# Kernel tuning notes

Measured on AMD Instinct MI355X. Metric: run time of the kernel, lower is better.

## Reference

```python
import jax, jax.numpy as jnp
import numpy as np

B, SQ, SK, DIMG, DTXT, D, H = 512, 49, 50, 2048, 768, 512, 4
DH = D // H
LN_EPS = 1e-5


def _proj_head(x, W1, b1, W2, b2, g, be):
    # Linear -> GELU -> Linear -> residual -> LayerNorm (dropout = eval/no-op)
    p = x @ W1 + b1
    h = jax.nn.gelu(p, approximate=False) @ W2 + b2 + p
    mu = h.mean(-1, keepdims=True)
    var = ((h - mu) ** 2).mean(-1, keepdims=True)
    return g * (h - mu) * jax.lax.rsqrt(var + LN_EPS) + be


def setup_inputs() -> dict:
    key = jax.random.key(0)
    ks = jax.random.split(key, 12)
    s = 0.02
    inp = {
        'image_features': jax.random.normal(ks[0], (B, DIMG, SQ), jnp.float32),
        'text_embeddings': jax.random.normal(ks[1], (B, SK, DTXT), jnp.float32),
        # image projection head (2048 -> 512)
        'Wi1': jax.random.normal(ks[2], (DIMG, D), jnp.float32) * s,
        'bi1': jnp.zeros((D,), jnp.float32),
        'Wi2': jax.random.normal(ks[3], (D, D), jnp.float32) * s,
        'bi2': jnp.zeros((D,), jnp.float32),
        'gi': jnp.ones((D,), jnp.float32),
        'bei': jnp.zeros((D,), jnp.float32),
        # text projection head (768 -> 512)
        'Wt1': jax.random.normal(ks[4], (DTXT, D), jnp.float32) * s,
        'bt1': jnp.zeros((D,), jnp.float32),
        'Wt2': jax.random.normal(ks[5], (D, D), jnp.float32) * s,
        'bt2': jnp.zeros((D,), jnp.float32),
        'gt': jnp.ones((D,), jnp.float32),
        'bet': jnp.zeros((D,), jnp.float32),
        # multihead cross-attention (embed_dim=512, 4 heads)
        'Wq': jax.random.normal(ks[6], (D, D), jnp.float32) * s,
        'bq': jnp.zeros((D,), jnp.float32),
        'Wk': jax.random.normal(ks[7], (D, D), jnp.float32) * s,
        'bk': jnp.zeros((D,), jnp.float32),
        'Wv': jax.random.normal(ks[8], (D, D), jnp.float32) * s,
        'bv': jnp.zeros((D,), jnp.float32),
        'Wo': jax.random.normal(ks[9], (D, D), jnp.float32) * s,
        'bo': jnp.zeros((D,), jnp.float32),
    }
    return inp


def reference(image_features, text_embeddings,
              Wi1, bi1, Wi2, bi2, gi, bei,
              Wt1, bt1, Wt2, bt2, gt, bet,
              Wq, bq, Wk, bk, Wv, bv, Wo, bo):
    img = jnp.transpose(image_features, (0, 2, 1))          # [B,SQ,2048]
    pi = _proj_head(img, Wi1, bi1, Wi2, bi2, gi, bei)        # [B,SQ,D]
    pt = _proj_head(text_embeddings, Wt1, bt1, Wt2, bt2, gt, bet)  # [B,SK,D]

    # cross attention: query = image tokens, key/value = text tokens
    q = (pi @ Wq + bq).reshape(B, SQ, H, DH)
    k = (pt @ Wk + bk).reshape(B, SK, H, DH)
    v = (pt @ Wv + bv).reshape(B, SK, H, DH)
    scores = jnp.einsum('bqhd,bkhd->bhqk', q, k) * (1.0 / np.sqrt(DH))
    a = jax.nn.softmax(scores, axis=-1)                      # [B,H,SQ,SK]
    o = jnp.einsum('bhqk,bkhd->bqhd', a, v).reshape(B, SQ, D)
    attn_output = o @ Wo + bo                                # [B,SQ,D]
    attn_weights = a.mean(axis=1)                            # torch MHA averages heads

    avg_attn = attn_output.mean(axis=1)                      # AdaptiveAvgPool1d(1) over SQ
    cls = pt[:, 0, :]                                        # [B,D]

    # cosine-similarity matrix: one normalize + matmul replaces B*B kernel launches
    n1 = avg_attn / jnp.linalg.norm(avg_attn, axis=-1, keepdims=True)
    n2 = cls / jnp.linalg.norm(cls, axis=-1, keepdims=True)
    score = n1 @ n2.T                                        # [B,B]
    return (score, attn_output, attn_weights, pi, pt)
```

## Files before the change

### kernel.cpp

```cpp
#include <hip/hip_runtime.h>
#include <math.h>

#define B_    512
#define SQ_   49
#define SK_   50
#define DIMG_ 2048
#define DTXT_ 768
#define D_    512
#define H_    4
#define DH_   128

#define SCORE_OFF 0
#define AO_OFF    262144
#define AW_OFF    13107200
#define PI_OFF    14361600
#define PT_OFF    27206656

typedef unsigned short bfbits;
typedef __attribute__((ext_vector_type(8))) short short8;
typedef __attribute__((ext_vector_type(4))) float floatx4;

static __device__ __forceinline__ bfbits f2bf(float f) {
    union { float f; unsigned u; } a; a.f = f;
    return (bfbits)((a.u + 0x7fffu + ((a.u >> 16) & 1u)) >> 16);
}
static __device__ __forceinline__ float bf2f(bfbits b) {
    union { unsigned u; float f; } a; a.u = ((unsigned)b) << 16;
    return a.f;
}
static __device__ __forceinline__ float gelu_exact(float x) {
    return 0.5f * x * (1.0f + erff(x * 0.70710678118654752f));
}

__global__ __launch_bounds__(256) void wcast_t(
    const float* __restrict__ W, bfbits* __restrict__ Wt, int K, int N)
{
    __shared__ float t[32][33];
    const int k0 = blockIdx.x * 32, n0 = blockIdx.y * 32;
    const int tx = threadIdx.x & 31, ty = threadIdx.x >> 5;
    #pragma unroll
    for (int i = 0; i < 32; i += 8)
        t[ty + i][tx] = W[(size_t)(k0 + ty + i) * N + n0 + tx];
    __syncthreads();
    #pragma unroll
    for (int i = 0; i < 32; i += 8)
        Wt[(size_t)(n0 + ty + i) * K + k0 + tx] = f2bf(t[tx][ty + i]);
}

__global__ __launch_bounds__(256) void img_t(
    const float* __restrict__ img, bfbits* __restrict__ A)
{
    __shared__ float t[64][50];
    const int b = blockIdx.y, k0 = blockIdx.x * 64;
    const float* src = img + (size_t)b * (DIMG_ * SQ_) + (size_t)k0 * SQ_;
    for (int e = threadIdx.x; e < 64 * 49; e += 256) {
        int kl = e / 49, s = e - kl * 49;
        t[kl][s] = src[kl * 49 + s];
    }
    __syncthreads();
    bfbits* dst = A + (size_t)b * SQ_ * DIMG_ + k0;
    for (int e = threadIdx.x; e < 49 * 64; e += 256) {
        int s = e >> 6, kl = e & 63;
        dst[(size_t)s * DIMG_ + kl] = f2bf(t[kl][s]);
    }
}

__global__ __launch_bounds__(256) void cast4(
    const float* __restrict__ x, bfbits* __restrict__ y, int n4)
{
    int i = blockIdx.x * 256 + threadIdx.x;
    if (i < n4) {
        float4 v = ((const float4*)x)[i];
        ushort4 u;
        u.x = f2bf(v.x); u.y = f2bf(v.y); u.z = f2bf(v.z); u.w = f2bf(v.w);
        ((ushort4*)y)[i] = u;
    }
}

template<bool RES, bool GELU, bool WF32, bool WBF>
__global__ __launch_bounds__(256) void gemm_bf16(
    const bfbits* __restrict__ A, const bfbits* __restrict__ Bt,
    const float* __restrict__ bias, const float* res,
    float* Cf, bfbits* __restrict__ Cb, int M, int K)
{
    constexpr int N = 512;
    __shared__ __attribute__((aligned(16))) bfbits As[128 * 32];
    __shared__ __attribute__((aligned(16))) bfbits Bs[128 * 32];
    const int tid  = threadIdx.x;
    const int wave = tid >> 6, lane = tid & 63;
    const int m0 = blockIdx.y * 128, n0 = blockIdx.x * 128;
    const int wm = (wave >> 1) * 64, wn = (wave & 1) * 64;
    const int lr = lane & 15, quad = lane >> 4;

    floatx4 acc[4][4];
    #pragma unroll
    for (int i = 0; i < 4; ++i)
        #pragma unroll
        for (int j = 0; j < 4; ++j) acc[i][j] = 0.0f;

    const int srow = lane >> 2;
    const int skof = (lane & 3) * 8;

    for (int k0 = 0; k0 < K; k0 += 32) {
        #pragma unroll
        for (int i = 0; i < 2; ++i) {
            const int c = wave * 2 + i;
            const int row = c * 16 + srow;
            const bfbits* ga = A + (size_t)(m0 + row) * K + k0 + skof;
            const bfbits* gb = Bt + (size_t)(n0 + row) * K + k0 + skof;
            __builtin_amdgcn_global_load_lds(
                (const __attribute__((address_space(1))) void*)ga,
                (__attribute__((address_space(3))) void*)(As + c * 512), 16, 0, 0);
            __builtin_amdgcn_global_load_lds(
                (const __attribute__((address_space(1))) void*)gb,
                (__attribute__((address_space(3))) void*)(Bs + c * 512), 16, 0, 0);
        }
        __syncthreads();

        short8 af[4], bfv[4];
        #pragma unroll
        for (int i = 0; i < 4; ++i) {
            af[i]  = *(const short8*)(As + (wm + i * 16 + lr) * 32 + quad * 8);
            bfv[i] = *(const short8*)(Bs + (wn + i * 16 + lr) * 32 + quad * 8);
        }
        #pragma unroll
        for (int i = 0; i < 4; ++i)
            #pragma unroll
            for (int j = 0; j < 4; ++j)
                acc[i][j] = __builtin_amdgcn_mfma_f32_16x16x32_bf16(
                    af[i], bfv[j], acc[i][j], 0, 0, 0);
        __syncthreads();
    }

    #pragma unroll
    for (int i = 0; i < 4; ++i) {
        #pragma unroll
        for (int j = 0; j < 4; ++j) {
            const int gc = n0 + wn + j * 16 + lr;
            const float bv = bias[gc];
            #pragma unroll
            for (int r = 0; r < 4; ++r) {
                const int gm = m0 + wm + i * 16 + quad * 4 + r;
                float v = acc[i][j][r] + bv;
                if (RES) v += res[(size_t)gm * N + gc];
                if (WF32) Cf[(size_t)gm * N + gc] = v;
                if (GELU) Cb[(size_t)gm * N + gc] = f2bf(gelu_exact(v));
                else if (WBF) Cb[(size_t)gm * N + gc] = f2bf(v);
            }
        }
    }
}

__global__ __launch_bounds__(256) void ln2_kernel(
    const float* __restrict__ h, const float* __restrict__ g,
    const float* __restrict__ be, float* __restrict__ outf,
    bfbits* __restrict__ outb)
{
    __shared__ float red[256];
    const int row = blockIdx.x;
    const int tid = threadIdx.x;
    float v0 = h[(size_t)row * D_ + tid];
    float v1 = h[(size_t)row * D_ + 256 + tid];
    red[tid] = v0 + v1;
    __syncthreads();
    for (int s = 128; s > 0; s >>= 1) {
        if (tid < s) red[tid] += red[tid + s];
        __syncthreads();
    }
    float mu = red[0] * (1.0f / 512.0f);
    __syncthreads();
    float d0 = v0 - mu, d1 = v1 - mu;
    red[tid] = d0 * d0 + d1 * d1;
    __syncthreads();
    for (int s = 128; s > 0; s >>= 1) {
        if (tid < s) red[tid] += red[tid + s];
        __syncthreads();
    }
    float var = red[0] * (1.0f / 512.0f);
    float sc = rsqrtf(var + 1e-5f);
    float o0 = g[tid] * d0 * sc + be[tid];
    float o1 = g[256 + tid] * d1 * sc + be[256 + tid];
    outf[(size_t)row * D_ + tid]       = o0;
    outf[(size_t)row * D_ + 256 + tid] = o1;
    outb[(size_t)row * D_ + tid]       = f2bf(o0);
    outb[(size_t)row * D_ + 256 + tid] = f2bf(o1);
}

__global__ __launch_bounds__(256) void attn_kernel(
    const bfbits* __restrict__ q, const bfbits* __restrict__ k,
    const bfbits* __restrict__ v, bfbits* __restrict__ o,
    float* __restrict__ aw)
{
    constexpr int ROWF = 69;
    __shared__ float sc[H_][SQ_ * ROWF];
    const int b = blockIdx.x;
    const int tid = threadIdx.x;
    const int h = tid >> 6, lane = tid & 63;
    const int lr = lane & 15, g = lane >> 4;

    const bfbits* kb = k + ((size_t)b * SK_) * D_ + h * DH_;
    const bfbits* qb = q + ((size_t)b * SQ_) * D_ + h * DH_;

    floatx4 acc[4][4];
    #pragma unroll
    for (int mi = 0; mi < 4; ++mi)
        #pragma unroll
        for (int ni = 0; ni < 4; ++ni) acc[mi][ni] = 0.0f;

    #pragma unroll
    for (int ks = 0; ks < 4; ++ks) {
        short8 afr[4], bfr[4];
        #pragma unroll
        for (int mi = 0; mi < 4; ++mi)
            afr[mi] = *(const short8*)(kb + (size_t)(mi * 16 + lr) * D_ + ks * 32 + g * 8);
        #pragma unroll
        for (int ni = 0; ni < 4; ++ni)
            bfr[ni] = *(const short8*)(qb + (size_t)(ni * 16 + lr) * D_ + ks * 32 + g * 8);
        #pragma unroll
        for (int mi = 0; mi < 4; ++mi)
            #pragma unroll
            for (int ni = 0; ni < 4; ++ni)
                acc[mi][ni] = __builtin_amdgcn_mfma_f32_16x16x32_bf16(
                    afr[mi], bfr[ni], acc[mi][ni], 0, 0, 0);
    }

    const float scale = 0.08838834764831845f;
    #pragma unroll
    for (int ni = 0; ni < 4; ++ni) {
        const int qi = ni * 16 + lr;
        float mx = -1e30f;
        #pragma unroll
        for (int mi = 0; mi < 4; ++mi)
            #pragma unroll
            for (int r = 0; r < 4; ++r) {
                const int ki = mi * 16 + g * 4 + r;
                float s = (ki < SK_) ? acc[mi][ni][r] * scale : -1e30f;
                acc[mi][ni][r] = s;
                mx = fmaxf(mx, s);
            }
        mx = fmaxf(mx, __shfl_xor(mx, 16));
        mx = fmaxf(mx, __shfl_xor(mx, 32));
        float sum = 0.f;
        #pragma unroll
        for (int mi = 0; mi < 4; ++mi)
            #pragma unroll
            for (int r = 0; r < 4; ++r) {
                float ev = __expf(acc[mi][ni][r] - mx);
                acc[mi][ni][r] = ev;
                sum += ev;
            }
        sum += __shfl_xor(sum, 16);
        sum += __shfl_xor(sum, 32);
        const float inv = 1.0f / sum;
        if (qi < SQ_) {
            #pragma unroll
            for (int mi = 0; mi < 4; ++mi) {
                float4 w;
                w.x = acc[mi][ni][0] * inv;
                w.y = acc[mi][ni][1] * inv;
                w.z = acc[mi][ni][2] * inv;
                w.w = acc[mi][ni][3] * inv;
                *(float4*)&sc[h][qi * ROWF + mi * 16 + g * 4] = w;
            }
        }
    }
    __syncthreads();

    for (int e = tid; e < SQ_ * SK_; e += 256) {
        int qi = e / SK_, ki = e - qi * SK_;
        const int off = qi * ROWF + ki;
        aw[(size_t)b * (SQ_ * SK_) + e] =
            0.25f * (sc[0][off] + sc[1][off] + sc[2][off] + sc[3][off]);
    }

    const bfbits* vb = v + ((size_t)b * SK_) * D_ + h * DH_;
    bfbits* ob = o + ((size_t)b * SQ_) * D_ + h * DH_;
    for (int e = lane; e < SQ_ * 16; e += 64) {
        const int qi = e >> 4, dc = e & 15;
        const float* sr = &sc[h][qi * ROWF];
        float s[8] = {0.f, 0.f, 0.f, 0.f, 0.f, 0.f, 0.f, 0.f};
        for (int ki = 0; ki < SK_; ++ki) {
            const float a = sr[ki];
            short8 u = *(const short8*)(vb + (size_t)ki * D_ + dc * 8);
            #pragma unroll
            for (int j = 0; j < 8; ++j)
                s[j] = fmaf(a, bf2f((bfbits)u[j]), s[j]);
        }
        short8 ov;
        #pragma unroll
        for (int j = 0; j < 8; ++j) ov[j] = (short)f2bf(s[j]);
        *(short8*)(ob + (size_t)qi * D_ + dc * 8) = ov;
    }
}

__global__ __launch_bounds__(256) void norm_kernel(
    const float* __restrict__ ao, const float* __restrict__ pt,
    float* __restrict__ n1, float* __restrict__ n2)
{
    __shared__ float red[256];
    const int b = blockIdx.x, tid = threadIdx.x;
    float s0 = 0.f, s1 = 0.f;
    for (int s = 0; s < SQ_; ++s) {
        s0 += ao[((size_t)(b * SQ_ + s)) * D_ + tid];
        s1 += ao[((size_t)(b * SQ_ + s)) * D_ + 256 + tid];
    }
    s0 *= (1.0f / 49.0f);
    s1 *= (1.0f / 49.0f);
    red[tid] = s0 * s0 + s1 * s1;
    __syncthreads();
    for (int st = 128; st > 0; st >>= 1) {
        if (tid < st) red[tid] += red[tid + st];
        __syncthreads();
    }
    float inv = rsqrtf(red[0]);
    __syncthreads();
    n1[(size_t)b * D_ + tid] = s0 * inv;
    n1[(size_t)b * D_ + 256 + tid] = s1 * inv;

    float c0 = pt[((size_t)(b * SK_)) * D_ + tid];
    float c1 = pt[((size_t)(b * SK_)) * D_ + 256 + tid];
    red[tid] = c0 * c0 + c1 * c1;
    __syncthreads();
    for (int st = 128; st > 0; st >>= 1) {
        if (tid < st) red[tid] += red[tid + st];
        __syncthreads();
    }
    float inv2 = rsqrtf(red[0]);
    n2[(size_t)b * D_ + tid] = c0 * inv2;
    n2[(size_t)b * D_ + 256 + tid] = c1 * inv2;
}

__global__ __launch_bounds__(256) void score_gemm(
    const float* __restrict__ A, const float* __restrict__ Bm,
    float* __restrict__ C)
{
    const int BM = 64, BN = 64, BK = 16, Kt = 512, Nt = 512;
    __shared__ float As[BK][BM + 1];
    __shared__ float Bs[BK][BN + 1];
    const int tid = threadIdx.x;
    const int m0 = blockIdx.y * BM, n0 = blockIdx.x * BN;
    const int tc = tid & 15, tr = tid >> 4;
    float acc[4][4] = {};
    for (int k0 = 0; k0 < Kt; k0 += BK) {
        #pragma unroll
        for (int i = 0; i < 4; ++i) {
            int idx = tid + i * 256;
            int m = idx >> 4, kk = idx & 15;
            As[kk][m] = A[(size_t)(m0 + m) * Kt + k0 + kk];
            Bs[kk][m] = Bm[(size_t)(n0 + m) * Kt + k0 + kk];
        }
        __syncthreads();
        #pragma unroll
        for (int kk = 0; kk < BK; ++kk) {
            float a4[4], b4[4];
            #pragma unroll
            for (int i = 0; i < 4; ++i) a4[i] = As[kk][tr * 4 + i];
            #pragma unroll
            for (int j = 0; j < 4; ++j) b4[j] = Bs[kk][tc * 4 + j];
            #pragma unroll
            for (int i = 0; i < 4; ++i)
                #pragma unroll
                for (int j = 0; j < 4; ++j)
                    acc[i][j] = fmaf(a4[i], b4[j], acc[i][j]);
        }
        __syncthreads();
    }
    #pragma unroll
    for (int i = 0; i < 4; ++i)
        #pragma unroll
        for (int j = 0; j < 4; ++j)
            C[(size_t)(m0 + tr * 4 + i) * Nt + n0 + tc * 4 + j] = acc[i][j];
}

extern "C" void kernel_launch(void* const* d_in, const int* in_sizes, int n_in,
                              void* d_out, int out_size, void* d_ws, size_t ws_size,
                              hipStream_t stream)
{
    const float* img = (const float*)d_in[0];
    const float* txt = (const float*)d_in[1];
    const float* Wi1 = (const float*)d_in[2];  const float* bi1 = (const float*)d_in[3];
    const float* Wi2 = (const float*)d_in[4];  const float* bi2 = (const float*)d_in[5];
    const float* gi  = (const float*)d_in[6];  const float* bei = (const float*)d_in[7];
    const float* Wt1 = (const float*)d_in[8];  const float* bt1 = (const float*)d_in[9];
    const float* Wt2 = (const float*)d_in[10]; const float* bt2 = (const float*)d_in[11];
    const float* gt  = (const float*)d_in[12]; const float* bet = (const float*)d_in[13];
    const float* Wq  = (const float*)d_in[14]; const float* bq  = (const float*)d_in[15];
    const float* Wk  = (const float*)d_in[16]; const float* bk  = (const float*)d_in[17];
    const float* Wv  = (const float*)d_in[18]; const float* bv  = (const float*)d_in[19];
    const float* Wo  = (const float*)d_in[20]; const float* bo  = (const float*)d_in[21];
    float* out = (float*)d_out;

    bfbits* Wi1T = (bfbits*)d_ws;
    bfbits* Wi2T = Wi1T + 1048576;
    bfbits* Wt1T = Wi2T + 262144;
    bfbits* Wt2T = Wt1T + 393216;
    bfbits* WqT  = Wt2T + 262144;
    bfbits* WkT  = WqT  + 262144;
    bfbits* WvT  = WkT  + 262144;
    bfbits* WoT  = WvT  + 262144;
    bfbits* R1   = WoT  + 262144;
    bfbits* Aimg = R1;
    bfbits* Atxt = R1;
    bfbits* Qbf  = R1 + 20000000;
    bfbits* Kbf  = R1 + 33200000;
    float*  R2   = (float*)(R1 + 51380224);
    bfbits* Vbf  = (bfbits*)R2;
    bfbits* R3   = (bfbits*)(R2 + 13107200);
    bfbits* Obf  = R3;
    bfbits* PiBf = R3 + 13107200;
    bfbits* PtBf = PiBf + 12845056;
    float*  n1   = (float*)(PtBf + 13107200);
    float*  n2   = n1 + 262144;

    const int MI = B_ * SQ_;
    const int MT = B_ * SK_;
    dim3 blk(256);

    wcast_t<<<dim3(DIMG_ / 32, D_ / 32), blk, 0, stream>>>(Wi1, Wi1T, DIMG_, D_);
    wcast_t<<<dim3(D_ / 32, D_ / 32),    blk, 0, stream>>>(Wi2, Wi2T, D_, D_);
    wcast_t<<<dim3(DTXT_ / 32, D_ / 32), blk, 0, stream>>>(Wt1, Wt1T, DTXT_, D_);
    wcast_t<<<dim3(D_ / 32, D_ / 32),    blk, 0, stream>>>(Wt2, Wt2T, D_, D_);
    wcast_t<<<dim3(D_ / 32, D_ / 32),    blk, 0, stream>>>(Wq, WqT, D_, D_);
    wcast_t<<<dim3(D_ / 32, D_ / 32),    blk, 0, stream>>>(Wk, WkT, D_, D_);
    wcast_t<<<dim3(D_ / 32, D_ / 32),    blk, 0, stream>>>(Wv, WvT, D_, D_);
    wcast_t<<<dim3(D_ / 32, D_ / 32),    blk, 0, stream>>>(Wo, WoT, D_, D_);

    img_t<<<dim3(DIMG_ / 64, B_), blk, 0, stream>>>(img, Aimg);
    gemm_bf16<false, true, true, true><<<dim3(4, MI / 128), blk, 0, stream>>>(
        Aimg, Wi1T, bi1, nullptr, R2, R3, MI, DIMG_);
    gemm_bf16<true, false, true, false><<<dim3(4, MI / 128), blk, 0, stream>>>(
        R3, Wi2T, bi2, R2, R2, nullptr, MI, D_);
    ln2_kernel<<<dim3(MI), blk, 0, stream>>>(R2, gi, bei, out + PI_OFF, PiBf);

    cast4<<<dim3((MT * DTXT_ / 4 + 255) / 256), blk, 0, stream>>>(txt, Atxt, MT * DTXT_ / 4);
    gemm_bf16<false, true, true, true><<<dim3(4, MT / 128), blk, 0, stream>>>(
        Atxt, Wt1T, bt1, nullptr, R2, R3, MT, DTXT_);
    gemm_bf16<true, false, true, false><<<dim3(4, MT / 128), blk, 0, stream>>>(
        R3, Wt2T, bt2, R2, R2, nullptr, MT, D_);
    ln2_kernel<<<dim3(MT), blk, 0, stream>>>(R2, gt, bet, out + PT_OFF, PtBf);

    gemm_bf16<false, false, false, true><<<dim3(4, MI / 128), blk, 0, stream>>>(
        PiBf, WqT, bq, nullptr, nullptr, Qbf, MI, D_);
    gemm_bf16<false, false, false, true><<<dim3(4, MT / 128), blk, 0, stream>>>(
        PtBf, WkT, bk, nullptr, nullptr, Kbf, MT, D_);
    gemm_bf16<false, false, false, true><<<dim3(4, MT / 128), blk, 0, stream>>>(
        PtBf, WvT, bv, nullptr, nullptr, Vbf, MT, D_);

    attn_kernel<<<dim3(B_), blk, 0, stream>>>(Qbf, Kbf, Vbf, Obf, out + AW_OFF);

    gemm_bf16<false, false, true, false><<<dim3(4, MI / 128), blk, 0, stream>>>(
        Obf, WoT, bo, nullptr, out + AO_OFF, nullptr, MI, D_);

    norm_kernel<<<dim3(B_), blk, 0, stream>>>(out + AO_OFF, out + PT_OFF, n1, n2);
    score_gemm<<<dim3(8, 8), blk, 0, stream>>>(n1, n2, out + SCORE_OFF);
}
```

Baseline: 1.092 ms.

## Double-buffer GEMM LDS tiles and remap blocks across XCDs

The bf16 MFMA GEMM now keeps two LDS buffers for A and B. It issues the global-to-LDS loads for the next K-tile before computing on the current one, so it needs one barrier per iteration instead of two. Launches switch to a 1-D grid, and the block index is permuted so that neighbouring logical tiles land on the same XCD chiplet, which is meant to improve L2 reuse of the shared A rows and weight columns. The cost is twice the LDS per block, which may reduce occupancy. The remap also assumes the grid size divides evenly by 8, which holds for these shapes.

After: 1.049 ms. 4.0% less time.

```diff
diff --git a/kernel.cpp b/kernel.cpp
--- a/kernel.cpp
+++ b/kernel.cpp
@@ -84,11 +84,17 @@
     float* Cf, bfbits* __restrict__ Cb, int M, int K)
 {
     constexpr int N = 512;
-    __shared__ __attribute__((aligned(16))) bfbits As[128 * 32];
-    __shared__ __attribute__((aligned(16))) bfbits Bs[128 * 32];
+    __shared__ __attribute__((aligned(16))) bfbits As[2][128 * 32];
+    __shared__ __attribute__((aligned(16))) bfbits Bs[2][128 * 32];
     const int tid  = threadIdx.x;
     const int wave = tid >> 6, lane = tid & 63;
-    const int m0 = blockIdx.y * 128, n0 = blockIdx.x * 128;
+
+    const int nwg = gridDim.x;
+    const int o = blockIdx.x;
+    const int qch = nwg >> 3;
+    const int lg = (o & 7) * qch + (o >> 3);
+    const int m0 = (lg >> 2) * 128, n0 = (lg & 3) * 128;
+
     const int wm = (wave >> 1) * 64, wn = (wave & 1) * 64;
     const int lr = lane & 15, quad = lane >> 4;
 
@@ -101,7 +107,7 @@
     const int srow = lane >> 2;
     const int skof = (lane & 3) * 8;
 
-    for (int k0 = 0; k0 < K; k0 += 32) {
+    auto stage = [&](int buf, int k0) {
         #pragma unroll
         for (int i = 0; i < 2; ++i) {
             const int c = wave * 2 + i;
@@ -110,18 +116,25 @@
             const bfbits* gb = Bt + (size_t)(n0 + row) * K + k0 + skof;
             __builtin_amdgcn_global_load_lds(
                 (const __attribute__((address_space(1))) void*)ga,
-                (__attribute__((address_space(3))) void*)(As + c * 512), 16, 0, 0);
+                (__attribute__((address_space(3))) void*)(&As[buf][c * 512]), 16, 0, 0);
             __builtin_amdgcn_global_load_lds(
                 (const __attribute__((address_space(1))) void*)gb,
-                (__attribute__((address_space(3))) void*)(Bs + c * 512), 16, 0, 0);
-        }
-        __syncthreads();
+                (__attribute__((address_space(3))) void*)(&Bs[buf][c * 512]), 16, 0, 0);
+        }
+    };
+
+    const int nt = K >> 5;
+    stage(0, 0);
+    __syncthreads();
+    int cur = 0;
+    for (int t = 0; t < nt; ++t) {
+        if (t + 1 < nt) stage(cur ^ 1, (t + 1) * 32);
 
         short8 af[4], bfv[4];
         #pragma unroll
         for (int i = 0; i < 4; ++i) {
-            af[i]  = *(const short8*)(As + (wm + i * 16 + lr) * 32 + quad * 8);
-            bfv[i] = *(const short8*)(Bs + (wn + i * 16 + lr) * 32 + quad * 8);
+            af[i]  = *(const short8*)(&As[cur][(wm + i * 16 + lr) * 32 + quad * 8]);
+            bfv[i] = *(const short8*)(&Bs[cur][(wn + i * 16 + lr) * 32 + quad * 8]);
         }
         #pragma unroll
         for (int i = 0; i < 4; ++i)
@@ -129,7 +142,9 @@
             for (int j = 0; j < 4; ++j)
                 acc[i][j] = __builtin_amdgcn_mfma_f32_16x16x32_bf16(
                     af[i], bfv[j], acc[i][j], 0, 0, 0);
-        __syncthreads();
+
+        __syncthreads();
+        cur ^= 1;
     }
 
     #pragma unroll
@@ -426,29 +441,29 @@
     wcast_t<<<dim3(D_ / 32, D_ / 32),    blk, 0, stream>>>(Wo, WoT, D_, D_);
 
     img_t<<<dim3(DIMG_ / 64, B_), blk, 0, stream>>>(img, Aimg);
-    gemm_bf16<false, true, true, true><<<dim3(4, MI / 128), blk, 0, stream>>>(
+    gemm_bf16<false, true, true, true><<<dim3(4 * (MI / 128)), blk, 0, stream>>>(
         Aimg, Wi1T, bi1, nullptr, R2, R3, MI, DIMG_);
-    gemm_bf16<true, false, true, false><<<dim3(4, MI / 128), blk, 0, stream>>>(
+    gemm_bf16<true, false, true, false><<<dim3(4 * (MI / 128)), blk, 0, stream>>>(
         R3, Wi2T, bi2, R2, R2, nullptr, MI, D_);
     ln2_kernel<<<dim3(MI), blk, 0, stream>>>(R2, gi, bei, out + PI_OFF, PiBf);
 
     cast4<<<dim3((MT * DTXT_ / 4 + 255) / 256), blk, 0, stream>>>(txt, Atxt, MT * DTXT_ / 4);
-    gemm_bf16<false, true, true, true><<<dim3(4, MT / 128), blk, 0, stream>>>(
+    gemm_bf16<false, true, true, true><<<dim3(4 * (MT / 128)), blk, 0, stream>>>(
         Atxt, Wt1T, bt1, nullptr, R2, R3, MT, DTXT_);
-    gemm_bf16<true, false, true, false><<<dim3(4, MT / 128), blk, 0, stream>>>(
+    gemm_bf16<true, false, true, false><<<dim3(4 * (MT / 128)), blk, 0, stream>>>(
         R3, Wt2T, bt2, R2, R2, nullptr, MT, D_);
     ln2_kernel<<<dim3(MT), blk, 0, stream>>>(R2, gt, bet, out + PT_OFF, PtBf);
 
-    gemm_bf16<false, false, false, true><<<dim3(4, MI / 128), blk, 0, stream>>>(
+    gemm_bf16<false, false, false, true><<<dim3(4 * (MI / 128)), blk, 0, stream>>>(
         PiBf, WqT, bq, nullptr, nullptr, Qbf, MI, D_);
-    gemm_bf16<false, false, false, true><<<dim3(4, MT / 128), blk, 0, stream>>>(
+    gemm_bf16<false, false, false, true><<<dim3(4 * (MT / 128)), blk, 0, stream>>>(
         PtBf, WkT, bk, nullptr, nullptr, Kbf, MT, D_);
-    gemm_bf16<false, false, false, true><<<dim3(4, MT / 128), blk, 0, stream>>>(
+    gemm_bf16<false, false, false, true><<<dim3(4 * (MT / 128)), blk, 0, stream>>>(
         PtBf, WvT, bv, nullptr, nullptr, Vbf, MT, D_);
 
     attn_kernel<<<dim3(B_), blk, 0, stream>>>(Qbf, Kbf, Vbf, Obf, out + AW_OFF);
 
-    gemm_bf16<false, false, true, false><<<dim3(4, MI / 128), blk, 0, stream>>>(
+    gemm_bf16<false, false, true, false><<<dim3(4 * (MI / 128)), blk, 0, stream>>>(
         Obf, WoT, bo, nullptr, out + AO_OFF, nullptr, MI, D_);
 
     norm_kernel<<<dim3(B_), blk, 0, stream>>>(out + AO_OFF, out + PT_OFF, n1, n2);
```
